# Kernel tuning notes

Hardware: AMD Instinct MI355X
Metric: run time of the kernel (lower is better)

The kernel has to match this reference:

```python
import jax, jax.numpy as jnp
import numpy as np

B, NN, D = 16, 50, 400
H, DH = 20, 20
ATT_H = 128
NEWS = 20000
K = 10
STEPS, SLOTS = 6, 10
EPS = 1e-5


def _layer_norm(x, g, b):
    m = jnp.mean(x, -1, keepdims=True)
    v = jnp.mean(jnp.square(x - m), -1, keepdims=True)
    return (x - m) * jax.lax.rsqrt(v + EPS) * g + b


def setup_inputs():
    key = jax.random.key(0)
    ks = jax.random.split(key, 9)
    s = 1.0 / np.sqrt(D)
    return {
        "news_input": jax.random.normal(ks[0], (B, NN, D), jnp.float32),
        "outputs_table": jax.random.normal(ks[1], (NEWS, K, D), jnp.float32) * 0.1,
        "Wq": jax.random.normal(ks[2], (D, H * DH), jnp.float32) * s,
        "Wk": jax.random.normal(ks[3], (D, H * DH), jnp.float32) * s,
        "Wv": jax.random.normal(ks[4], (D, H * DH), jnp.float32) * s,
        "ln1_g": jnp.ones((D,), jnp.float32),
        "ln1_b": jnp.zeros((D,), jnp.float32),
        "fc1_w": jax.random.normal(ks[5], (D, ATT_H), jnp.float32) * s,
        "fc1_b": jnp.zeros((ATT_H,), jnp.float32),
        "fc2_w": jax.random.normal(ks[6], (ATT_H, 1), jnp.float32) * (1.0 / np.sqrt(ATT_H)),
        "fc2_b": jnp.zeros((1,), jnp.float32),
        "ln2_g": jnp.ones((D,), jnp.float32),
        "ln2_b": jnp.zeros((D,), jnp.float32),
        "click_history": jax.random.randint(ks[7], (B, NN), 1, NEWS + 1),
        "neighbor_table": jax.random.randint(ks[8], (NEWS + 1, K), 1, NEWS + 1),
        "mask": jnp.ones((B, 50 * SLOTS), jnp.int32),
    }


def _traverse(news_input, outputs_table, click_history, neighbor_table):
    # Vectorized form of the per-item 6-hop neighbor traversal.
    def step(carry, _):
        idx, dead = carry                                          # [B,N] int, [B,N] bool
        vg = outputs_table[idx - 1]                                # [B,N,K,D] gather
        scores = jnp.einsum('bnkd,bnd->bnk', vg, news_input)      # [B,N,K]
        mx_i = jnp.argmax(scores, -1)
        mx_v = jnp.take_along_axis(scores, mx_i[..., None], -1)[..., 0]
        nz = scores != 0
        any_nz = jnp.any(nz, -1)
        nz_i = jnp.argmax(jnp.where(nz, scores, -jnp.inf), -1)
        hop = (mx_v == 0) & jnp.logical_not(dead)                  # max score exactly 0 -> follow graph
        sel_i = jnp.where(hop & any_nz, nz_i, mx_i)
        new_dead = dead | (hop & jnp.logical_not(any_nz))
        nbr = jnp.take_along_axis(neighbor_table[idx], sel_i[..., None], -1)[..., 0]
        new_idx = jnp.where(hop & any_nz, nbr, idx)
        sel = jnp.take_along_axis(vg, sel_i[..., None, None], 2)[..., 0, :]
        sel = jnp.where(new_dead[..., None], 0.0, sel)
        return (new_idx, new_dead), sel

    init = (click_history, jnp.zeros(click_history.shape, bool))
    _, sels = jax.lax.scan(step, init, None, length=STEPS)         # [6,B,N,D]
    sels = jnp.moveaxis(sels, 0, 2)                                # [B,N,6,D]
    valid = jnp.any(news_input != 0, -1).astype(sels.dtype)        # skip all-zero news rows
    sels = sels * valid[..., None, None]
    res = jnp.pad(sels, ((0, 0), (0, 0), (0, SLOTS - STEPS), (0, 0)))
    if NN < 50:
        res = jnp.pad(res, ((0, 0), (0, 50 - NN), (0, 0), (0, 0)))
    return res                                                      # [B,50,10,D]


def _mha(x, mask, Wq, Wk, Wv):
    L = x.shape[1]
    q = (x @ Wq).reshape(-1, L, H, DH).transpose(0, 2, 1, 3)
    k = (x @ Wk).reshape(-1, L, H, DH).transpose(0, 2, 1, 3)
    v = (x @ Wv).reshape(-1, L, H, DH).transpose(0, 2, 1, 3)
    sc = jnp.einsum('bhqd,bhkd->bhqk', q, k) / np.float32(np.sqrt(DH))
    sc = jnp.where(mask[:, None, None, :] > 0, sc, -1e9)
    a = jax.nn.softmax(sc, -1)
    o = jnp.einsum('bhqk,bhkd->bhqd', a, v)
    return o.transpose(0, 2, 1, 3).reshape(-1, L, H * DH)


def _att_pool(x, mask, fc1_w, fc1_b, fc2_w, fc2_b):
    e = jnp.tanh(x @ fc1_w + fc1_b) @ fc2_w + fc2_b                # [B*50,10,1]
    e = jnp.where(mask[..., None] > 0, e, -1e9)
    a = jax.nn.softmax(e, 1)
    return jnp.sum(a * x, 1)


def reference(news_input, outputs_table, Wq, Wk, Wv, ln1_g, ln1_b,
              fc1_w, fc1_b, fc2_w, fc2_b, ln2_g, ln2_b,
              click_history, neighbor_table, mask):
    res = _traverse(news_input, outputs_table, click_history, neighbor_table)
    x = res.reshape(-1, 50 * SLOTS, D)
    x = _mha(x, mask, Wq, Wk, Wv)
    x = x.reshape(-1, SLOTS, D)
    x = _layer_norm(x, ln1_g, ln1_b)
    x = _att_pool(x, mask.reshape(-1, SLOTS), fc1_w, fc1_b, fc2_w, fc2_b)
    x = _layer_norm(x, ln2_g, ln2_b)
    return x.reshape(-1, 50, D)
```

## Files before the change

kernel.cpp:

```cpp
#include <hip/hip_runtime.h>
#include <hip/hip_bf16.h>
#include <math.h>

#define B 16
#define NN 50
#define D 400
#define H 20
#define DH 20
#define ATT_H 128
#define NEWS 20000
#define K 10
#define STEPS 6
#define SLOTS 10
#define L 500
#define EPS 1e-5f

#define XP 416
#define NC 1200

typedef short short4v __attribute__((ext_vector_type(4)));
typedef short short8 __attribute__((ext_vector_type(8)));
typedef float floatx4 __attribute__((ext_vector_type(4)));
typedef float floatx2 __attribute__((ext_vector_type(2)));

__device__ __forceinline__ short f2bf(float f) {
    __hip_bfloat16 h = __float2bfloat16(f);
    return *reinterpret_cast<short*>(&h);
}

__global__ __launch_bounds__(256) void k_prep(
    const float* __restrict__ news,
    const float* __restrict__ table,
    const int*   __restrict__ click,
    const int*   __restrict__ nbrt,
    const float* __restrict__ Wq, const float* __restrict__ Wk,
    const float* __restrict__ Wv,
    short* __restrict__ x,
    short* __restrict__ wT)
{
    __shared__ float ssc[K];

    int blk = blockIdx.x;
    int tid = threadIdx.x;

    if (blk >= B * NN) {
        int c = blk - B * NN;
        int z = c / 400, n = c % 400;
        const float* W = (z == 0) ? Wq : (z == 1) ? Wk : Wv;
        float sc = (z == 0) ? 0.22360679774997896f : 1.0f;
        for (int k = tid; k < XP; k += 256)
            wT[(size_t)c * XP + k] = (k < 400) ? f2bf(W[(size_t)k * 400 + n] * sc) : (short)0;
        return;
    }

    int item = blk;
    int b = item / NN, n = item % NN;
    int lane = tid & 63, w = tid >> 6;

    float nv[7];
    bool nzf = false;
    #pragma unroll
    for (int i = 0; i < 7; i++) {
        int d = lane + 64 * i;
        float v = (d < D) ? news[(size_t)item * D + d] : 0.0f;
        nv[i] = v;
        nzf |= (v != 0.0f);
    }
    float valid = __any(nzf) ? 1.0f : 0.0f;

    int idx = click[item];
    bool dead = false;
    short* xbase = x + (size_t)(b * L + n * SLOTS) * XP;

    for (int step = 0; step < STEPS; step++) {
        const float* tb = table + (size_t)(idx - 1) * K * D;
        for (int kk = w; kk < K; kk += 4) {
            float p = 0.0f;
            #pragma unroll
            for (int i = 0; i < 7; i++) {
                int d = lane + 64 * i;
                if (d < D) p += tb[kk * D + d] * nv[i];
            }
            #pragma unroll
            for (int off = 32; off > 0; off >>= 1) p += __shfl_xor(p, off);
            if (lane == 0) ssc[kk] = p;
        }
        __syncthreads();

        float scores[K];
        #pragma unroll
        for (int kk = 0; kk < K; kk++) scores[kk] = ssc[kk];

        int mx_i = 0; float mx_v = scores[0];
        #pragma unroll
        for (int kk = 1; kk < K; kk++)
            if (scores[kk] > mx_v) { mx_v = scores[kk]; mx_i = kk; }

        bool any_nz = false; int nz_i = 0; float nz_v = -INFINITY;
        #pragma unroll
        for (int kk = 0; kk < K; kk++) {
            if (scores[kk] != 0.0f) {
                if (!any_nz || scores[kk] > nz_v) { nz_v = scores[kk]; nz_i = kk; }
                any_nz = true;
            }
        }

        bool hop = (mx_v == 0.0f) && !dead;
        int sel_i = (hop && any_nz) ? nz_i : mx_i;
        bool new_dead = dead || (hop && !any_nz);
        int nbr = nbrt[(size_t)idx * K + sel_i];
        int new_idx = (hop && any_nz) ? nbr : idx;

        float scale = new_dead ? 0.0f : valid;
        const float* selrow = tb + (size_t)sel_i * D;
        short* xr = xbase + (size_t)step * XP;
        for (int d2 = tid; d2 < XP / 2; d2 += 256) {
            int d = d2 * 2;
            int pr = 0;
            if (d < D) {
                floatx2 fv = *(const floatx2*)&selrow[d];
                int lo = f2bf(fv[0] * scale) & 0xffff;
                int hi = f2bf(fv[1] * scale) & 0xffff;
                pr = lo | (hi << 16);
            }
            *(int*)&xr[d] = pr;
        }

        idx = new_idx; dead = new_dead;
        __syncthreads();
    }
    for (int s = STEPS; s < SLOTS; s++) {
        short* xr = xbase + (size_t)s * XP;
        for (int d8 = tid; d8 < XP / 8; d8 += 256) {
            int4 z = {0, 0, 0, 0};
            *(int4*)&xr[d8 * 8] = z;
        }
    }
}

#define BM 128
#define BN 128
#define BKK 32

__global__ __launch_bounds__(256) void k_qkv_mfma(
    const short* __restrict__ xg,
    const short* __restrict__ wT,
    short* __restrict__ c)
{
    __shared__ short xs[BM][BKK + 8];
    __shared__ short wt[BN][BKK + 8];

    int tid = threadIdx.x;
    int m0 = blockIdx.x * BM;
    int n0 = blockIdx.y * BN;
    int lane = tid & 63, w = tid >> 6;
    int wr = w >> 1, wc = w & 1;
    int quad = lane >> 4, l16 = lane & 15;

    floatx4 acc[4][4];
    #pragma unroll
    for (int i = 0; i < 4; i++)
        #pragma unroll
        for (int j = 0; j < 4; j++) acc[i][j] = (floatx4){0.f, 0.f, 0.f, 0.f};

    int xr = tid >> 1, xc = (tid & 1) * 16;
    bool xok = (m0 + xr) < 8000;
    bool wok = (n0 + xr) < NC;

    for (int k0 = 0; k0 < XP; k0 += BKK) {
        int4 xv0 = {0,0,0,0}, xv1 = {0,0,0,0}, wv0 = {0,0,0,0}, wv1 = {0,0,0,0};
        if (xok) {
            const int4* src = (const int4*)(xg + (size_t)(m0 + xr) * XP + k0 + xc);
            xv0 = src[0]; xv1 = src[1];
        }
        if (wok) {
            const int4* src = (const int4*)(wT + (size_t)(n0 + xr) * XP + k0 + xc);
            wv0 = src[0]; wv1 = src[1];
        }
        __syncthreads();
        *(int4*)&xs[xr][xc]     = xv0;
        *(int4*)&xs[xr][xc + 8] = xv1;
        *(int4*)&wt[xr][xc]     = wv0;
        *(int4*)&wt[xr][xc + 8] = wv1;
        __syncthreads();

        short8 a[4], bf[4];
        #pragma unroll
        for (int fi = 0; fi < 4; fi++)
            a[fi] = *(const short8*)&xs[wr * 64 + fi * 16 + l16][quad * 8];
        #pragma unroll
        for (int fj = 0; fj < 4; fj++)
            bf[fj] = *(const short8*)&wt[wc * 64 + fj * 16 + l16][quad * 8];
        #pragma unroll
        for (int fi = 0; fi < 4; fi++)
            #pragma unroll
            for (int fj = 0; fj < 4; fj++)
                acc[fi][fj] = __builtin_amdgcn_mfma_f32_16x16x32_bf16(
                    a[fi], bf[fj], acc[fi][fj], 0, 0, 0);
    }

    #pragma unroll
    for (int fi = 0; fi < 4; fi++) {
        int grow_base = m0 + wr * 64 + fi * 16 + quad * 4;
        #pragma unroll
        for (int fj = 0; fj < 4; fj++) {
            int gcol = n0 + wc * 64 + fj * 16 + l16;
            #pragma unroll
            for (int r = 0; r < 4; r++) {
                int grow = grow_base + r;
                if (grow < 8000 && gcol < NC)
                    c[(size_t)grow * NC + gcol] = f2bf(acc[fi][fj][r]);
            }
        }
    }
}

#define KSTR 24
#define VSTR 520
#define PSTR 40
#define QSPLIT 2

__global__ __launch_bounds__(256) void k_attn4(
    const short* __restrict__ qkv,
    const int* __restrict__ mask,
    float* __restrict__ o)
{
    __shared__ short sh[12288 + 21 * VSTR + 4 * 16 * PSTR + 512];
    short* VTb = sh + 12288;
    short* Pb  = VTb + 21 * VSTR;
    short* msk = Pb + 4 * 16 * PSTR;

    int part = blockIdx.x & (QSPLIT - 1);
    int bh = blockIdx.x >> 1;
    int b = bh / H, h = bh % H;
    int tid = threadIdx.x;
    int lane = tid & 63, w = tid >> 6;
    int quad = lane >> 4, l16 = lane & 15;

    for (int u = tid; u < 512 * (KSTR / 2); u += 256) {
        int j = u / (KSTR / 2), t = u % (KSTR / 2);
        int v = 0;
        if (j < L && t < DH / 2)
            v = *(const int*)(qkv + (size_t)(b * L + j) * NC + 400 + h * DH + 2 * t);
        *(int*)&sh[j * KSTR + 2 * t] = v;
    }
    for (int u = tid; u < L * (DH / 2); u += 256) {
        int j = u / (DH / 2), t = u % (DH / 2);
        int v = *(const int*)(qkv + (size_t)(b * L + j) * NC + 800 + h * DH + 2 * t);
        VTb[(2 * t) * VSTR + j]     = (short)(v & 0xffff);
        VTb[(2 * t + 1) * VSTR + j] = (short)((unsigned)v >> 16);
    }
    for (int j = tid; j < 512; j += 256) {
        VTb[20 * VSTR + j] = (j < L) ? f2bf(1.0f) : (short)0;
        msk[j] = (j < L && mask[(size_t)b * L + j] > 0) ? f2bf(1.0f) : (short)0;
    }
    for (int i = tid; i < DH * 12; i += 256) {
        int d = i / 12, j = L + i % 12;
        VTb[d * VSTR + j] = 0;
    }
    __syncthreads();

    short* Pw = Pb + w * 16 * PSTR;
    short* pwr = Pw + l16 * PSTR;
    const short* prd = Pw + l16 * PSTR + quad * 8;
    const short* kA  = sh + quad * 8;
    const short* vA0 = VTb + l16 * VSTR;
    int r1 = 16 + l16; if (r1 > 20) r1 = 20;
    const short* vA1 = VTb + r1 * VSTR;

    for (int qt = part * 16 + w; qt < part * 16 + 16; qt += 4) {
        int qrow = qt * 16 + l16;
        const short* qp = qkv + (size_t)(b * L + (qrow < L ? qrow : 0)) * NC + h * DH;
        short8 aq = (short8)(short)0;
        if (quad < 2) {
            short4v a0 = *(const short4v*)(qp + quad * 8);
            short4v a1 = *(const short4v*)(qp + quad * 8 + 4);
            #pragma unroll
            for (int jj = 0; jj < 4; jj++) { aq[jj] = a0[jj]; aq[4 + jj] = a1[jj]; }
        } else if (quad == 2) {
            short4v a0 = *(const short4v*)(qp + 16);
            #pragma unroll
            for (int jj = 0; jj < 4; jj++) aq[jj] = a0[jj];
        }

        floatx4 O0 = (floatx4){0.f,0.f,0.f,0.f};
        floatx4 O1 = (floatx4){0.f,0.f,0.f,0.f};
        float mrun = -INFINITY;

        for (int jt = 0; jt < 16; jt++) {
            short8 ak0 = (short8)(short)0, ak1 = (short8)(short)0;
            if (quad < 3) {
                ak0 = *(const short8*)&kA[(jt * 32 + l16) * KSTR];
                ak1 = *(const short8*)&kA[(jt * 32 + 16 + l16) * KSTR];
            }
            floatx4 z = (floatx4){0.f,0.f,0.f,0.f};
            floatx4 s0 = __builtin_amdgcn_mfma_f32_16x16x32_bf16(ak0, aq, z, 0, 0, 0);
            floatx4 s1 = __builtin_amdgcn_mfma_f32_16x16x32_bf16(ak1, aq, z, 0, 0, 0);

            short4v mk0 = *(const short4v*)&msk[jt * 32 + quad * 4];
            short4v mk1 = *(const short4v*)&msk[jt * 32 + 16 + quad * 4];
            #pragma unroll
            for (int r = 0; r < 4; r++) {
                s0[r] = (mk0[r] != 0) ? s0[r] : -1e9f;
                s1[r] = (mk1[r] != 0) ? s1[r] : -1e9f;
            }

            float mt = fmaxf(fmaxf(fmaxf(s0[0], s0[1]), fmaxf(s0[2], s0[3])),
                             fmaxf(fmaxf(s1[0], s1[1]), fmaxf(s1[2], s1[3])));
            mt = fmaxf(mt, __shfl_xor(mt, 16));
            mt = fmaxf(mt, __shfl_xor(mt, 32));

            if (!__all(mt <= mrun)) {
                float mnew = fmaxf(mrun, mt);
                float alpha = __expf(mrun - mnew);
                mrun = mnew;
                #pragma unroll
                for (int r = 0; r < 4; r++) { O0[r] *= alpha; O1[r] *= alpha; }
            }

            short4v pk0, pk1;
            #pragma unroll
            for (int r = 0; r < 4; r++) {
                pk0[r] = f2bf(__expf(s0[r] - mrun));
                pk1[r] = f2bf(__expf(s1[r] - mrun));
            }
            *(short4v*)&pwr[quad * 4]      = pk0;
            *(short4v*)&pwr[16 + quad * 4] = pk1;

            short8 ap  = *(const short8*)prd;
            short8 va0 = *(const short8*)&vA0[jt * 32 + quad * 8];
            short8 va1 = *(const short8*)&vA1[jt * 32 + quad * 8];
            O0 = __builtin_amdgcn_mfma_f32_16x16x32_bf16(va0, ap, O0, 0, 0, 0);
            O1 = __builtin_amdgcn_mfma_f32_16x16x32_bf16(va1, ap, O1, 0, 0, 0);
        }

        float lsum = __shfl(O1[0], 16 + l16);
        float inv = 1.0f / lsum;
        int q = qt * 16 + l16;
        if (q < L) {
            float* op = o + (size_t)(b * L + q) * (H * DH) + h * DH;
            floatx4 v0;
            #pragma unroll
            for (int r = 0; r < 4; r++) v0[r] = O0[r] * inv;
            *(floatx4*)&op[quad * 4] = v0;
            if (quad == 0) {
                floatx4 v1;
                #pragma unroll
                for (int r = 0; r < 4; r++) v1[r] = O1[r] * inv;
                *(floatx4*)&op[16] = v1;
            }
        }
    }
}

__global__ __launch_bounds__(256) void k_pool(
    const float* __restrict__ o,
    const float* __restrict__ ln1g, const float* __restrict__ ln1b,
    const float* __restrict__ fc1w, const float* __restrict__ fc1b,
    const float* __restrict__ fc2w, const float* __restrict__ fc2b,
    const float* __restrict__ ln2g, const float* __restrict__ ln2b,
    const int* __restrict__ mask,
    float* __restrict__ out)
{
    __shared__ float xt[SLOTS][D];
    __shared__ float hv[SLOTS * ATT_H];
    __shared__ float es[SLOTS];
    __shared__ float red[8];

    int g = blockIdx.x;
    int tid = threadIdx.x;
    int lane = tid & 63, w = tid >> 6;

    const float* xg = o + (size_t)g * SLOTS * D;

    for (int s = w; s < SLOTS; s += 4) {
        const float* xr = xg + (size_t)s * D;
        float vbuf[7];
        float sum = 0.0f, sq = 0.0f;
        #pragma unroll
        for (int i = 0; i < 7; i++) {
            int d = lane + 64 * i;
            float v = (d < D) ? xr[d] : 0.0f;
            vbuf[i] = v; sum += v; sq += v * v;
        }
        #pragma unroll
        for (int off = 32; off > 0; off >>= 1) {
            sum += __shfl_xor(sum, off);
            sq  += __shfl_xor(sq, off);
        }
        float mean = sum / (float)D;
        float var = sq / (float)D - mean * mean;
        float rs = rsqrtf(var + EPS);
        #pragma unroll
        for (int i = 0; i < 7; i++) {
            int d = lane + 64 * i;
            if (d < D) xt[s][d] = (vbuf[i] - mean) * rs * ln1g[d] + ln1b[d];
        }
    }
    __syncthreads();

    {
        int jh = tid & 127;
        int s0 = tid >> 7;
        float hs[5];
        #pragma unroll
        for (int jj = 0; jj < 5; jj++) hs[jj] = fc1b[jh];
        for (int d = 0; d < D; d += 4) {
            floatx4 xv0 = *(const floatx4*)&xt[s0 + 0][d];
            floatx4 xv1 = *(const floatx4*)&xt[s0 + 2][d];
            floatx4 xv2 = *(const floatx4*)&xt[s0 + 4][d];
            floatx4 xv3 = *(const floatx4*)&xt[s0 + 6][d];
            floatx4 xv4 = *(const floatx4*)&xt[s0 + 8][d];
            #pragma unroll
            for (int dd = 0; dd < 4; dd++) {
                float fw = fc1w[(size_t)(d + dd) * ATT_H + jh];
                hs[0] += xv0[dd] * fw;
                hs[1] += xv1[dd] * fw;
                hs[2] += xv2[dd] * fw;
                hs[3] += xv3[dd] * fw;
                hs[4] += xv4[dd] * fw;
            }
        }
        float f2 = fc2w[jh];
        #pragma unroll
        for (int jj = 0; jj < 5; jj++)
            hv[(s0 + 2 * jj) * ATT_H + jh] = tanhf(hs[jj]) * f2;
    }
    __syncthreads();

    for (int s = w; s < SLOTS; s += 4) {
        float p = hv[s * ATT_H + lane] + hv[s * ATT_H + lane + 64];
        #pragma unroll
        for (int off = 32; off > 0; off >>= 1) p += __shfl_xor(p, off);
        if (lane == 0) es[s] = p + fc2b[0];
    }
    __syncthreads();

    float ev[SLOTS];
    float emax = -INFINITY;
    #pragma unroll
    for (int s = 0; s < SLOTS; s++) {
        float e = (mask[(size_t)g * SLOTS + s] > 0) ? es[s] : -1e9f;
        ev[s] = e;
        if (e > emax) emax = e;
    }
    float esum = 0.0f;
    #pragma unroll
    for (int s = 0; s < SLOTS; s++) { ev[s] = __expf(ev[s] - emax); esum += ev[s]; }
    float einv = 1.0f / esum;

    int d0 = tid, d1 = tid + 256;
    float p0 = 0.0f, p1 = 0.0f;
    #pragma unroll
    for (int s = 0; s < SLOTS; s++) {
        p0 += ev[s] * xt[s][d0];
        if (d1 < D) p1 += ev[s] * xt[s][d1];
    }
    p0 *= einv; p1 *= einv;

    float sum = p0 + ((d1 < D) ? p1 : 0.0f);
    float sq  = p0 * p0 + ((d1 < D) ? p1 * p1 : 0.0f);
    #pragma unroll
    for (int off = 32; off > 0; off >>= 1) {
        sum += __shfl_xor(sum, off);
        sq  += __shfl_xor(sq, off);
    }
    if (lane == 0) { red[w] = sum; red[4 + w] = sq; }
    __syncthreads();
    float tsum = red[0] + red[1] + red[2] + red[3];
    float tsq  = red[4] + red[5] + red[6] + red[7];
    float mean = tsum / (float)D;
    float var = tsq / (float)D - mean * mean;
    float rs = rsqrtf(var + EPS);

    float* og = out + (size_t)g * D;
    og[d0] = (p0 - mean) * rs * ln2g[d0] + ln2b[d0];
    if (d1 < D) og[d1] = (p1 - mean) * rs * ln2g[d1] + ln2b[d1];
}

extern "C" void kernel_launch(void* const* d_in, const int* in_sizes, int n_in,
                              void* d_out, int out_size, void* d_ws, size_t ws_size,
                              hipStream_t stream) {
    const float* news  = (const float*)d_in[0];
    const float* table = (const float*)d_in[1];
    const float* Wq    = (const float*)d_in[2];
    const float* Wk    = (const float*)d_in[3];
    const float* Wv    = (const float*)d_in[4];
    const float* ln1g  = (const float*)d_in[5];
    const float* ln1b  = (const float*)d_in[6];
    const float* fc1w  = (const float*)d_in[7];
    const float* fc1b  = (const float*)d_in[8];
    const float* fc2w  = (const float*)d_in[9];
    const float* fc2b  = (const float*)d_in[10];
    const float* ln2g  = (const float*)d_in[11];
    const float* ln2b  = (const float*)d_in[12];
    const int* click   = (const int*)d_in[13];
    const int* nbrt    = (const int*)d_in[14];
    const int* mask    = (const int*)d_in[15];
    float* out = (float*)d_out;

    char* p = (char*)d_ws;
    short* xbf = (short*)p;  p += (size_t)8000 * XP * sizeof(short);
    short* wT  = (short*)p;  p += (size_t)NC * XP * sizeof(short);
    short* qkv = (short*)p;  p += (size_t)8000 * NC * sizeof(short);
    float* ob  = (float*)p;

    k_prep<<<dim3(B * NN + NC), dim3(256), 0, stream>>>(
        news, table, click, nbrt, Wq, Wk, Wv, xbf, wT);
    k_qkv_mfma<<<dim3((8000 + BM - 1) / BM, (NC + BN - 1) / BN), dim3(256), 0, stream>>>(
        xbf, wT, qkv);
    k_attn4<<<dim3(B * H * QSPLIT), dim3(256), 0, stream>>>(qkv, mask, ob);
    k_pool<<<dim3(B * NN), dim3(256), 0, stream>>>(ob, ln1g, ln1b, fc1w, fc1b, fc2w, fc2b,
                                                   ln2g, ln2b, mask, out);
}
```

Baseline: 510.2 us.

## Tile weight transpose through LDS, prefetch neighbors, pool two groups per block

The weight-transpose blocks now load 16 columns by 400 rows into a shared-memory tile with coalesced reads and write contiguous bf16 rows, cutting the transpose from 1200 to 75 blocks. The neighbor-table row is read into shared memory early in each traversal step, so the dependent global load after the argmax is replaced by an LDS lookup. The pooling kernel handles two groups per block, so each fc1 weight load is reused across 10 slots instead of 5. This raises register use and the pooling block's shared-memory footprint, and halves the number of pooling blocks.

After: 515.7 us. No clear change (+1.1%).

```diff
diff --git a/kernel.cpp b/kernel.cpp
--- a/kernel.cpp
+++ b/kernel.cpp
@@ -17,6 +17,7 @@
 
 #define XP 416
 #define NC 1200
+#define WTB 75
 
 typedef short short4v __attribute__((ext_vector_type(4)));
 typedef short short8 __attribute__((ext_vector_type(8)));
@@ -39,17 +40,29 @@
     short* __restrict__ wT)
 {
     __shared__ float ssc[K];
+    __shared__ int   snbr[K];
 
     int blk = blockIdx.x;
     int tid = threadIdx.x;
 
     if (blk >= B * NN) {
-        int c = blk - B * NN;
-        int z = c / 400, n = c % 400;
+        __shared__ float wtile[16][401];
+        int blk2 = blk - B * NN;
+        int z = blk2 / 25, nt = blk2 % 25;
+        int n0 = nt * 16;
         const float* W = (z == 0) ? Wq : (z == 1) ? Wk : Wv;
         float sc = (z == 0) ? 0.22360679774997896f : 1.0f;
-        for (int k = tid; k < XP; k += 256)
-            wT[(size_t)c * XP + k] = (k < 400) ? f2bf(W[(size_t)k * 400 + n] * sc) : (short)0;
+        int kk = tid >> 4, noff = tid & 15;
+        for (int k0 = 0; k0 < 400; k0 += 16)
+            wtile[noff][k0 + kk] = W[(size_t)(k0 + kk) * 400 + n0 + noff];
+        __syncthreads();
+        int c0 = z * 400 + n0;
+        for (int r = 0; r < 16; r++) {
+            short* dst = wT + (size_t)(c0 + r) * XP;
+            dst[tid] = f2bf(wtile[r][tid] * sc);
+            int c2 = tid + 256;
+            if (c2 < XP) dst[c2] = (c2 < 400) ? f2bf(wtile[r][c2] * sc) : (short)0;
+        }
         return;
     }
 
@@ -74,6 +87,7 @@
 
     for (int step = 0; step < STEPS; step++) {
         const float* tb = table + (size_t)(idx - 1) * K * D;
+        if (tid < K) snbr[tid] = nbrt[(size_t)idx * K + tid];
         for (int kk = w; kk < K; kk += 4) {
             float p = 0.0f;
             #pragma unroll
@@ -108,7 +122,7 @@
         bool hop = (mx_v == 0.0f) && !dead;
         int sel_i = (hop && any_nz) ? nz_i : mx_i;
         bool new_dead = dead || (hop && !any_nz);
-        int nbr = nbrt[(size_t)idx * K + sel_i];
+        int nbr = snbr[sel_i];
         int new_idx = (hop && any_nz) ? nbr : idx;
 
         float scale = new_dead ? 0.0f : valid;
@@ -362,18 +376,18 @@
     const int* __restrict__ mask,
     float* __restrict__ out)
 {
-    __shared__ float xt[SLOTS][D];
-    __shared__ float hv[SLOTS * ATT_H];
-    __shared__ float es[SLOTS];
-    __shared__ float red[8];
-
-    int g = blockIdx.x;
+    __shared__ float xt[2 * SLOTS][D];
+    __shared__ float hv[2 * SLOTS * ATT_H];
+    __shared__ float es[2 * SLOTS];
+    __shared__ float red[2][8];
+
+    int g0 = blockIdx.x * 2;
     int tid = threadIdx.x;
     int lane = tid & 63, w = tid >> 6;
 
-    const float* xg = o + (size_t)g * SLOTS * D;
-
-    for (int s = w; s < SLOTS; s += 4) {
+    const float* xg = o + (size_t)g0 * SLOTS * D;
+
+    for (int s = w; s < 2 * SLOTS; s += 4) {
         const float* xr = xg + (size_t)s * D;
         float vbuf[7];
         float sum = 0.0f, sq = 0.0f;
@@ -401,34 +415,30 @@
 
     {
         int jh = tid & 127;
-        int s0 = tid >> 7;
-        float hs[5];
-        #pragma unroll
-        for (int jj = 0; jj < 5; jj++) hs[jj] = fc1b[jh];
+        int grp = tid >> 7;
+        float hs[SLOTS];
+        #pragma unroll
+        for (int s = 0; s < SLOTS; s++) hs[s] = fc1b[jh];
         for (int d = 0; d < D; d += 4) {
-            floatx4 xv0 = *(const floatx4*)&xt[s0 + 0][d];
-            floatx4 xv1 = *(const floatx4*)&xt[s0 + 2][d];
-            floatx4 xv2 = *(const floatx4*)&xt[s0 + 4][d];
-            floatx4 xv3 = *(const floatx4*)&xt[s0 + 6][d];
-            floatx4 xv4 = *(const floatx4*)&xt[s0 + 8][d];
+            floatx4 xv[SLOTS];
+            #pragma unroll
+            for (int s = 0; s < SLOTS; s++)
+                xv[s] = *(const floatx4*)&xt[grp * SLOTS + s][d];
             #pragma unroll
             for (int dd = 0; dd < 4; dd++) {
                 float fw = fc1w[(size_t)(d + dd) * ATT_H + jh];
-                hs[0] += xv0[dd] * fw;
-                hs[1] += xv1[dd] * fw;
-                hs[2] += xv2[dd] * fw;
-                hs[3] += xv3[dd] * fw;
-                hs[4] += xv4[dd] * fw;
+                #pragma unroll
+                for (int s = 0; s < SLOTS; s++) hs[s] += xv[s][dd] * fw;
             }
         }
         float f2 = fc2w[jh];
         #pragma unroll
-        for (int jj = 0; jj < 5; jj++)
-            hv[(s0 + 2 * jj) * ATT_H + jh] = tanhf(hs[jj]) * f2;
+        for (int s = 0; s < SLOTS; s++)
+            hv[(grp * SLOTS + s) * ATT_H + jh] = tanhf(hs[s]) * f2;
     }
     __syncthreads();
 
-    for (int s = w; s < SLOTS; s += 4) {
+    for (int s = w; s < 2 * SLOTS; s += 4) {
         float p = hv[s * ATT_H + lane] + hv[s * ATT_H + lane + 64];
         #pragma unroll
         for (int off = 32; off > 0; off >>= 1) p += __shfl_xor(p, off);
@@ -436,46 +446,48 @@
     }
     __syncthreads();
 
-    float ev[SLOTS];
-    float emax = -INFINITY;
-    #pragma unroll
-    for (int s = 0; s < SLOTS; s++) {
-        float e = (mask[(size_t)g * SLOTS + s] > 0) ? es[s] : -1e9f;
-        ev[s] = e;
-        if (e > emax) emax = e;
-    }
-    float esum = 0.0f;
-    #pragma unroll
-    for (int s = 0; s < SLOTS; s++) { ev[s] = __expf(ev[s] - emax); esum += ev[s]; }
-    float einv = 1.0f / esum;
-
-    int d0 = tid, d1 = tid + 256;
-    float p0 = 0.0f, p1 = 0.0f;
-    #pragma unroll
-    for (int s = 0; s < SLOTS; s++) {
-        p0 += ev[s] * xt[s][d0];
-        if (d1 < D) p1 += ev[s] * xt[s][d1];
-    }
-    p0 *= einv; p1 *= einv;
-
-    float sum = p0 + ((d1 < D) ? p1 : 0.0f);
-    float sq  = p0 * p0 + ((d1 < D) ? p1 * p1 : 0.0f);
-    #pragma unroll
-    for (int off = 32; off > 0; off >>= 1) {
-        sum += __shfl_xor(sum, off);
-        sq  += __shfl_xor(sq, off);
-    }
-    if (lane == 0) { red[w] = sum; red[4 + w] = sq; }
-    __syncthreads();
-    float tsum = red[0] + red[1] + red[2] + red[3];
-    float tsq  = red[4] + red[5] + red[6] + red[7];
-    float mean = tsum / (float)D;
-    float var = tsq / (float)D - mean * mean;
-    float rs = rsqrtf(var + EPS);
-
-    float* og = out + (size_t)g * D;
-    og[d0] = (p0 - mean) * rs * ln2g[d0] + ln2b[d0];
-    if (d1 < D) og[d1] = (p1 - mean) * rs * ln2g[d1] + ln2b[d1];
+    for (int g = 0; g < 2; g++) {
+        float ev[SLOTS];
+        float emax = -INFINITY;
+        #pragma unroll
+        for (int s = 0; s < SLOTS; s++) {
+            float e = (mask[(size_t)(g0 + g) * SLOTS + s] > 0) ? es[g * SLOTS + s] : -1e9f;
+            ev[s] = e;
+            if (e > emax) emax = e;
+        }
+        float esum = 0.0f;
+        #pragma unroll
+        for (int s = 0; s < SLOTS; s++) { ev[s] = __expf(ev[s] - emax); esum += ev[s]; }
+        float einv = 1.0f / esum;
+
+        int d0 = tid, d1 = tid + 256;
+        float p0 = 0.0f, p1 = 0.0f;
+        #pragma unroll
+        for (int s = 0; s < SLOTS; s++) {
+            p0 += ev[s] * xt[g * SLOTS + s][d0];
+            if (d1 < D) p1 += ev[s] * xt[g * SLOTS + s][d1];
+        }
+        p0 *= einv; p1 *= einv;
+
+        float sum = p0 + ((d1 < D) ? p1 : 0.0f);
+        float sq  = p0 * p0 + ((d1 < D) ? p1 * p1 : 0.0f);
+        #pragma unroll
+        for (int off = 32; off > 0; off >>= 1) {
+            sum += __shfl_xor(sum, off);
+            sq  += __shfl_xor(sq, off);
+        }
+        if (lane == 0) { red[g][w] = sum; red[g][4 + w] = sq; }
+        __syncthreads();
+        float tsum = red[g][0] + red[g][1] + red[g][2] + red[g][3];
+        float tsq  = red[g][4] + red[g][5] + red[g][6] + red[g][7];
+        float mean = tsum / (float)D;
+        float var = tsq / (float)D - mean * mean;
+        float rs = rsqrtf(var + EPS);
+
+        float* og = out + (size_t)(g0 + g) * D;
+        og[d0] = (p0 - mean) * rs * ln2g[d0] + ln2b[d0];
+        if (d1 < D) og[d1] = (p1 - mean) * rs * ln2g[d1] + ln2b[d1];
+    }
 }
 
 extern "C" void kernel_launch(void* const* d_in, const int* in_sizes, int n_in,
@@ -505,11 +517,11 @@
     short* qkv = (short*)p;  p += (size_t)8000 * NC * sizeof(short);
     float* ob  = (float*)p;
 
-    k_prep<<<dim3(B * NN + NC), dim3(256), 0, stream>>>(
+    k_prep<<<dim3(B * NN + WTB), dim3(256), 0, stream>>>(
         news, table, click, nbrt, Wq, Wk, Wv, xbf, wT);
     k_qkv_mfma<<<dim3((8000 + BM - 1) / BM, (NC + BN - 1) / BN), dim3(256), 0, stream>>>(
         xbf, wT, qkv);
     k_attn4<<<dim3(B * H * QSPLIT), dim3(256), 0, stream>>>(qkv, mask, ob);
-    k_pool<<<dim3(B * NN), dim3(256), 0, stream>>>(ob, ln1g, ln1b, fc1w, fc1b, fc2w, fc2b,
-                                                   ln2g, ln2b, mask, out);
+    k_pool<<<dim3(B * NN / 2), dim3(256), 0, stream>>>(ob, ln1g, ln1b, fc1w, fc1b,
+                                                       fc2w, fc2b, ln2g, ln2b, mask, out);
 }
```
